# Optimization experiments

Measured on AMD Instinct MI355X. Metric: run time of the kernel, lower is better.

## Reference

```python
import jax, jax.numpy as jnp
import numpy as np
import math

N_PARENT = 60000
CH = 64
BATCH = 2
GRID = 128          # parent voxels on even coords in [0, 256)^3
P_BIT = 0.33
LOG2E = math.log2(math.e)


def _key(b, x, y, z):
    # collision-free int64 key; +4 keeps shifted neighbor coords non-negative
    return ((np.asarray(b, np.int64) * 512 + (x + 4)) * 512 + (y + 4)) * 512 + (z + 4)


def _nbr(qc, tkeys, step):
    # 3x3x3 kernel offset map (torchsparse Conv3d k=3,s=1 at tensor stride `step`)
    so = np.argsort(tkeys)
    sk = tkeys[so]
    d = np.array([-step, 0, step], np.int64)
    offs = np.stack(np.meshgrid(d, d, d, indexing='ij'), -1).reshape(-1, 3)  # [27,3]
    q = _key(qc[:, 0:1], qc[:, 1:2] + offs[None, :, 0],
             qc[:, 2:3] + offs[None, :, 1], qc[:, 3:4] + offs[None, :, 2])
    pos = np.minimum(np.searchsorted(sk, q), len(sk) - 1)
    return np.where(sk[pos] == q, so[pos], -1).astype(np.int32)


def setup_inputs():
    rng = np.random.default_rng(0)
    half = N_PARENT // 2
    cs = []
    for b in range(BATCH):
        lin = rng.choice(GRID ** 3, half, replace=False)
        x, y, z = lin // (GRID * GRID), (lin // GRID) % GRID, lin % GRID
        cs.append(np.stack([np.full(half, b), 2 * x, 2 * y, 2 * z], 1).astype(np.int64))
    C = np.concatenate(cs, 0)                                  # [N,4] batch-major, stride-2 coords
    pkeys = _key(C[:, 0], C[:, 1], C[:, 2], C[:, 3])
    bits1 = rng.random((N_PARENT, 8)) < P_BIT                  # cur_bins[1].F occupancy bits
    bits1[~bits1.any(1), 0] = True
    pidx, bitj = np.nonzero(bits1)                             # row-major order == bool-mask gather order
    off = np.stack([(bitj >> 2) & 1, (bitj >> 1) & 1, bitj & 1], 1)
    CC = np.concatenate([C[pidx, :1], C[pidx, 1:] + off], 1)   # child coords, stride 1
    ckeys = _key(CC[:, 0], CC[:, 1], CC[:, 2], CC[:, 3])
    M = CC.shape[0]
    bits0 = rng.random((M, 8)) < P_BIT                         # cur_bins[0].F
    bits0[~bits0.any(1), 0] = True
    f32 = np.float32

    def lin_(fi, fo):
        return (rng.standard_normal((fi, fo)).astype(f32) / f32(np.sqrt(fi)),
                (rng.standard_normal(fo) * 0.01).astype(f32))

    def conv_(c, d):
        return (rng.standard_normal((27, c, d)).astype(f32) / f32(np.sqrt(27 * c)),
                (rng.standard_normal(d) * 0.01).astype(f32))

    W_dec, b_dec = lin_(CH + 8, CH)
    Wb1, bb1 = conv_(CH, CH)
    Wb2, bb2 = conv_(CH, CH)
    Wp0c, bp0c = conv_(CH, CH)
    Wp0l, bp0l = lin_(CH, CH * 8)
    Wp1c, bp1c = conv_(CH, CH)
    Wp1l, bp1l = lin_(CH, 255)
    a = lambda: np.full((1,), 0.25, f32)   # torch nn.PReLU default
    inp = dict(
        rec_F=rng.standard_normal((N_PARENT, CH)).astype(f32),
        bins1_F=bits1.astype(f32),
        points_num=np.bincount(CC[:, 0], minlength=BATCH).astype(f32),
        W_dec=W_dec, b_dec=b_dec, a_dec=a(),
        Wb1=Wb1, bb1=bb1, ab1=a(), Wb2=Wb2, bb2=bb2, ab2=a(),
        Wp0c=Wp0c, bp0c=bp0c, ap0=a(), Wp0l=Wp0l, bp0l=bp0l,
        Wp1c=Wp1c, bp1c=bp1c, ap1=a(), Wp1l=Wp1l, bp1l=bp1l,
        nbr_rec=_nbr(C, pkeys, 2),
        nbr_child=_nbr(CC, ckeys, 1),
        child_pidx=pidx.astype(np.int32), child_bit=bitj.astype(np.int32),
        bins0=bits0.astype(np.int32),
        oct_kernel=np.arange(7, -1, -1, dtype=np.int32),
        ref_batch=CC[:, 0].astype(np.int32),
    )
    return {k: jnp.asarray(v) for k, v in inp.items()}


def _prelu(x, a):
    return jnp.where(x >= 0, x, a * x)


def _sconv(x, nbr, W, b):
    # sparse 3x3x3 conv: out[i] = b + sum_k W[k]^T x[nbr[i,k]] over existing neighbors
    valid = nbr >= 0
    idx = jnp.maximum(nbr, 0)
    out = jnp.zeros((x.shape[0], W.shape[-1]), x.dtype)
    for k in range(W.shape[0]):  # 27 fixed kernel offsets
        xk = jnp.where(valid[:, k:k + 1], x[idx[:, k]], 0.0)
        out = out + xk @ W[k]
    return out + b


def _forward(rec_F, bins1_F, points_num, W_dec, b_dec, a_dec, Wb1, bb1, ab1, Wb2, bb2, ab2,
             Wp0c, bp0c, ap0, Wp0l, bp0l, Wp1c, bp1c, ap1, Wp1l, bp1l,
             nbr_rec, nbr_child, child_pidx, child_bit, bins0, oct_kernel, ref_batch):
    # pred_steps==2: embed is identity -> embed_f == cur_bins[1].F
    x = jnp.concatenate([rec_F, bins1_F], 1)                  # [N, CH+8]
    h = _prelu(x @ W_dec + b_dec, a_dec)
    # Block: conv-PReLU-conv + residual, PReLU
    t = _prelu(_sconv(h, nbr_rec, Wb1, bb1), ab1)
    t = _sconv(t, nbr_rec, Wb2, bb2) + h
    y = _prelu(t, ab2)                                        # cur_rec.F after dec
    # pred[0]
    p = _prelu(_sconv(y, nbr_rec, Wp0c, bp0c), ap0)
    l8 = (p @ Wp0l + bp0l).reshape(-1, 8, rec_F.shape[1])     # [N,8,CH]
    # bool-mask gather reshape(N,8,CH)[cur_bins[-1].F] -> [M,CH]
    g = l8[child_pidx, child_bit]
    # pred[-1]
    q = _prelu(_sconv(g, nbr_child, Wp1c, bp1c), ap1)
    logits = q @ Wp1l + bp1l                                  # [M,255]
    oct = jnp.sum(bins0 << oct_kernel, axis=1) - 1            # bit-packed targets in [0,254]
    logp = jax.nn.log_softmax(logits, axis=-1)
    ce = -jnp.take_along_axis(logp, oct[:, None], axis=1)[:, 0]
    scattered = points_num[ref_batch]                         # searchsorted+loop == per-batch broadcast
    loss = (ce / scattered).sum() * (LOG2E / points_num.shape[0])
    return y, loss


def reference(rec_F, bins1_F, points_num, W_dec, b_dec, a_dec, Wb1, bb1, ab1, Wb2, bb2, ab2,
              Wp0c, bp0c, ap0, Wp0l, bp0l, Wp1c, bp1c, ap1, Wp1l, bp1l,
              nbr_rec, nbr_child, child_pidx, child_bit, bins0, oct_kernel, ref_batch):
    return _forward(rec_F, bins1_F, points_num, W_dec, b_dec, a_dec, Wb1, bb1, ab1, Wb2, bb2, ab2,
                    Wp0c, bp0c, ap0, Wp0l, bp0l, Wp1c, bp1c, ap1, Wp1l, bp1l,
                    nbr_rec, nbr_child, child_pidx, child_bit, bins0, oct_kernel, ref_batch)
```

## Files before the change

kernel.cpp:

```cpp
#include <hip/hip_runtime.h>
#include <hip/hip_bf16.h>

typedef __hip_bfloat16 bf16;
typedef __attribute__((ext_vector_type(8))) short bf16x8v;
typedef __attribute__((ext_vector_type(4))) float f32x4v;

__device__ __forceinline__ float b2f(bf16 v) { return __bfloat162float(v); }
__device__ __forceinline__ float lo16(unsigned int u) {
    union { unsigned int i; float f; } x; x.i = u << 16; return x.f;
}
__device__ __forceinline__ float hi16(unsigned int u) {
    union { unsigned int i; float f; } x; x.i = u & 0xffff0000u; return x.f;
}
template<typename T>
__device__ __forceinline__ void load8(const T* p, float o[8]);
template<>
__device__ __forceinline__ void load8<bf16>(const bf16* p, float o[8]) {
    uint4 v = *reinterpret_cast<const uint4*>(p);
    o[0] = lo16(v.x); o[1] = hi16(v.x);
    o[2] = lo16(v.y); o[3] = hi16(v.y);
    o[4] = lo16(v.z); o[5] = hi16(v.z);
    o[6] = lo16(v.w); o[7] = hi16(v.w);
}
template<>
__device__ __forceinline__ void load8<float>(const float* p, float o[8]) {
    float4 a = reinterpret_cast<const float4*>(p)[0];
    float4 b = reinterpret_cast<const float4*>(p)[1];
    o[0] = a.x; o[1] = a.y; o[2] = a.z; o[3] = a.w;
    o[4] = b.x; o[5] = b.y; o[6] = b.z; o[7] = b.w;
}

__global__ void k_code(float* __restrict__ out, size_t n, float code)
{
    size_t i0 = (size_t)blockIdx.x * blockDim.x + threadIdx.x;
    size_t stride = (size_t)gridDim.x * blockDim.x;
    for (size_t i = i0; i < n; i += stride) out[i] = code;
}

__global__ __launch_bounds__(256) void k_wt(
    const float* __restrict__ W0, const float* __restrict__ W1,
    const float* __restrict__ W2, const float* __restrict__ W3,
    bf16* __restrict__ WT)
{
    __shared__ float L[64 * 65];
    int wb = blockIdx.x / 27, k = blockIdx.x % 27;
    const float* src = (wb == 0 ? W0 : wb == 1 ? W1 : wb == 2 ? W2 : W3) + (size_t)k * 4096;
    int tid = threadIdx.x;
    #pragma unroll
    for (int i = 0; i < 16; ++i) {
        int e = i * 256 + tid;
        L[(e >> 6) * 65 + (e & 63)] = src[e];
    }
    __syncthreads();
    bf16* dst = WT + ((size_t)wb * 27 + k) * 4096;
    #pragma unroll
    for (int i = 0; i < 16; ++i) {
        int e = i * 256 + tid;
        dst[e] = __float2bfloat16(L[(e & 63) * 65 + (e >> 6)]);
    }
}

__global__ __launch_bounds__(256) void k_wt5(
    const float* __restrict__ W, bf16* __restrict__ WT5)
{
    int c = threadIdx.x;
    #pragma unroll
    for (int j = 0; j < 64; ++j) {
        float v = (c < 255) ? W[(size_t)j * 255 + c] : 0.f;
        WT5[(size_t)c * 64 + j] = __float2bfloat16(v);
    }
}

__global__ __launch_bounds__(256) void k_dec(
    const float* __restrict__ rec, const float* __restrict__ bins,
    const float* __restrict__ W, const float* __restrict__ b, const float* __restrict__ a,
    bf16* __restrict__ h, int N)
{
    __shared__ float Wl[72 * 64];
    int tid = threadIdx.x;
    for (int i = tid; i < 72 * 64; i += 256) Wl[i] = W[i];
    int c = tid & 63, w = tid >> 6;
    float bc = b[c];
    float av = a[0];
    __syncthreads();
    int base = blockIdx.x * 32 + w * 8;
    for (int rr = 0; rr < 8; ++rr) {
        int row = base + rr;
        if (row >= N) break;
        float acc = bc;
        float xv[8];
        #pragma unroll
        for (int j8 = 0; j8 < 8; ++j8) {
            load8(rec + (size_t)row * 64 + j8 * 8, xv);
            int j = j8 * 8;
            #pragma unroll
            for (int t = 0; t < 8; ++t) acc += xv[t] * Wl[(j + t) * 64 + c];
        }
        load8(bins + (size_t)row * 8, xv);
        #pragma unroll
        for (int t = 0; t < 8; ++t) acc += xv[t] * Wl[(64 + t) * 64 + c];
        float v = acc >= 0.f ? acc : av * acc;
        h[(size_t)row * 64 + c] = __float2bfloat16(v);
    }
}

template<int G, bool RES, bool OUTF>
__global__ __launch_bounds__(256) void k_sconv_mfma(
    const bf16* __restrict__ x, const int* __restrict__ nbr,
    const bf16* __restrict__ WT,
    const float* __restrict__ bias, const float* __restrict__ a,
    const bf16* __restrict__ res, bf16* __restrict__ out,
    float* __restrict__ outf, int N)
{
    int tid = threadIdx.x;
    int lane = tid & 63;
    int wv = tid >> 6;
    int l15 = lane & 15;
    int lq = lane >> 4;
    int rowbase = blockIdx.x * (64 * G) + wv * (16 * G);

    f32x4v acc[G][4];
    #pragma unroll
    for (int g = 0; g < G; ++g)
        #pragma unroll
        for (int ct = 0; ct < 4; ++ct) acc[g][ct] = (f32x4v){0.f, 0.f, 0.f, 0.f};

    for (int k = 0; k < 27; ++k) {
        int idx[G];
        int anyl = 0;
        #pragma unroll
        for (int g = 0; g < G; ++g) {
            int row = rowbase + g * 16 + l15;
            idx[g] = (row < N) ? nbr[(size_t)row * 27 + k] : -1;
            anyl |= (idx[g] >= 0) ? 1 : 0;
        }
        if (!__any(anyl)) continue;

        bf16x8v bfr[4][2];
        const bf16* wk = WT + (size_t)k * 4096;
        #pragma unroll
        for (int ct = 0; ct < 4; ++ct) {
            const bf16* wr = wk + (ct * 16 + l15) * 64 + lq * 8;
            bfr[ct][0] = *reinterpret_cast<const bf16x8v*>(wr);
            bfr[ct][1] = *reinterpret_cast<const bf16x8v*>(wr + 32);
        }
        #pragma unroll
        for (int g = 0; g < G; ++g) {
            if (!__any(idx[g] >= 0)) continue;
            bf16x8v a0 = (bf16x8v){0,0,0,0,0,0,0,0};
            bf16x8v a1 = (bf16x8v){0,0,0,0,0,0,0,0};
            if (idx[g] >= 0) {
                const bf16* xr = x + (size_t)idx[g] * 64 + lq * 8;
                a0 = *reinterpret_cast<const bf16x8v*>(xr);
                a1 = *reinterpret_cast<const bf16x8v*>(xr + 32);
            }
            #pragma unroll
            for (int ct = 0; ct < 4; ++ct) {
                acc[g][ct] = __builtin_amdgcn_mfma_f32_16x16x32_bf16(a0, bfr[ct][0], acc[g][ct], 0, 0, 0);
                acc[g][ct] = __builtin_amdgcn_mfma_f32_16x16x32_bf16(a1, bfr[ct][1], acc[g][ct], 0, 0, 0);
            }
        }
    }

    float av = a[0];
    float bs[4];
    #pragma unroll
    for (int ct = 0; ct < 4; ++ct) bs[ct] = bias[ct * 16 + l15];
    #pragma unroll
    for (int g = 0; g < G; ++g) {
        #pragma unroll
        for (int r = 0; r < 4; ++r) {
            int row = rowbase + g * 16 + lq * 4 + r;
            if (row >= N) continue;
            #pragma unroll
            for (int ct = 0; ct < 4; ++ct) {
                int col = ct * 16 + l15;
                float v = acc[g][ct][r] + bs[ct];
                if (RES) v += b2f(res[(size_t)row * 64 + col]);
                v = v >= 0.f ? v : av * v;
                out[(size_t)row * 64 + col] = __float2bfloat16(v);
                if (OUTF) outf[(size_t)row * 64 + col] = v;
            }
        }
    }
}

__global__ __launch_bounds__(256) void k_p0l(
    const bf16* __restrict__ p, const float* __restrict__ W, const float* __restrict__ b,
    const int* __restrict__ pidx, const int* __restrict__ bitj,
    bf16* __restrict__ g, int M)
{
    int tid = threadIdx.x;
    int c = tid & 63, w = tid >> 6;
    int base = blockIdx.x * 32 + w * 8;
    for (int rr = 0; rr < 8; ++rr) {
        int m = base + rr;
        if (m >= M) break;
        int pi = pidx[m];
        int bt = bitj[m];
        int col = bt * 64 + c;
        float acc = b[col];
        float xv[8];
        #pragma unroll
        for (int j8 = 0; j8 < 8; ++j8) {
            load8(p + (size_t)pi * 64 + j8 * 8, xv);
            int j = j8 * 8;
            #pragma unroll
            for (int t = 0; t < 8; ++t)
                acc += xv[t] * W[(size_t)(j + t) * 512 + col];
        }
        g[(size_t)m * 64 + c] = __float2bfloat16(acc);
    }
}

__global__ __launch_bounds__(256) void k_loss_mfma(
    const bf16* __restrict__ q, const bf16* __restrict__ WT5,
    const float* __restrict__ b,
    const int* __restrict__ bins0, const int* __restrict__ octk,
    const int* __restrict__ ref_batch, const float* __restrict__ pn,
    float* __restrict__ accum, int M)
{
    int tid = threadIdx.x;
    int lane = tid & 63;
    int wv = tid >> 6;
    int l15 = lane & 15;
    int lq = lane >> 4;

    bf16x8v bfr[16][2];
    #pragma unroll
    for (int ct = 0; ct < 16; ++ct) {
        const bf16* wr = WT5 + (size_t)(ct * 16 + l15) * 64 + lq * 8;
        bfr[ct][0] = *reinterpret_cast<const bf16x8v*>(wr);
        bfr[ct][1] = *reinterpret_cast<const bf16x8v*>(wr + 32);
    }
    float bs[16];
    #pragma unroll
    for (int ct = 0; ct < 16; ++ct) bs[ct] = (ct * 16 + l15 < 255) ? b[ct * 16 + l15] : 0.f;
    int ok[8];
    #pragma unroll
    for (int j = 0; j < 8; ++j) ok[j] = octk[j];

    float local = 0.f;
    int tiles = (M + 15) / 16;
    int waveId = blockIdx.x * 4 + wv;
    int nWaves = gridDim.x * 4;

    for (int t = waveId; t < tiles; t += nWaves) {
        int rowbase = t * 16;
        int arow = rowbase + l15;
        bf16x8v a0 = (bf16x8v){0,0,0,0,0,0,0,0};
        bf16x8v a1 = (bf16x8v){0,0,0,0,0,0,0,0};
        if (arow < M) {
            const bf16* xr = q + (size_t)arow * 64 + lq * 8;
            a0 = *reinterpret_cast<const bf16x8v*>(xr);
            a1 = *reinterpret_cast<const bf16x8v*>(xr + 32);
        }
        f32x4v acc[16];
        #pragma unroll
        for (int ct = 0; ct < 16; ++ct) {
            f32x4v z = (f32x4v){0.f, 0.f, 0.f, 0.f};
            z = __builtin_amdgcn_mfma_f32_16x16x32_bf16(a0, bfr[ct][0], z, 0, 0, 0);
            z = __builtin_amdgcn_mfma_f32_16x16x32_bf16(a1, bfr[ct][1], z, 0, 0, 0);
            acc[ct] = z;
        }
        #pragma unroll
        for (int ct = 0; ct < 16; ++ct) {
            #pragma unroll
            for (int r = 0; r < 4; ++r) acc[ct][r] += bs[ct];
        }
        #pragma unroll
        for (int r = 0; r < 4; ++r) {
            int row = rowbase + lq * 4 + r;
            bool rv = (row < M);
            int rowc = rv ? row : 0;
            float mx = -1e30f;
            #pragma unroll
            for (int ct = 0; ct < 16; ++ct) {
                float v = acc[ct][r];
                if (ct == 15 && l15 == 15) v = -1e30f;
                mx = fmaxf(mx, v);
            }
            #pragma unroll
            for (int s = 1; s < 16; s <<= 1) mx = fmaxf(mx, __shfl_xor(mx, s, 64));
            float se = 0.f;
            #pragma unroll
            for (int ct = 0; ct < 16; ++ct) {
                if (ct == 15 && l15 == 15) continue;
                se += __expf(acc[ct][r] - mx);
            }
            #pragma unroll
            for (int s = 1; s < 16; s <<= 1) se += __shfl_xor(se, s, 64);
            int oct = 0;
            #pragma unroll
            for (int j = 0; j < 8; ++j) oct += bins0[(size_t)rowc * 8 + j] << ok[j];
            oct -= 1;
            int cts = oct >> 4;
            float cand = acc[0][r];
            #pragma unroll
            for (int ct = 1; ct < 16; ++ct) cand = (cts == ct) ? acc[ct][r] : cand;
            float lo = __shfl(cand, lq * 16 + (oct & 15), 64);
            if (rv && l15 == 0) {
                float ce = mx + __logf(se) - lo;
                local += ce / pn[ref_batch[row]];
            }
        }
    }
    #pragma unroll
    for (int s = 32; s > 0; s >>= 1) local += __shfl_xor(local, s, 64);
    if (lane == 0) atomicAdd(accum, local);
}

__global__ void k_finish(const float* __restrict__ accum, float* __restrict__ outf, int BATCH)
{
    if (threadIdx.x == 0 && blockIdx.x == 0)
        outf[0] = accum[0] * 1.4426950408889634f / (float)BATCH;
}

extern "C" void kernel_launch(void* const* d_in, const int* in_sizes, int n_in,
                              void* d_out, int out_size, void* d_ws, size_t ws_size,
                              hipStream_t stream)
{
    const float* rec_F   = (const float*)d_in[0];
    const float* bins1_F = (const float*)d_in[1];
    const float* pn      = (const float*)d_in[2];
    const float* W_dec   = (const float*)d_in[3];
    const float* b_dec   = (const float*)d_in[4];
    const float* a_dec   = (const float*)d_in[5];
    const float* Wb1     = (const float*)d_in[6];
    const float* bb1     = (const float*)d_in[7];
    const float* ab1     = (const float*)d_in[8];
    const float* Wb2     = (const float*)d_in[9];
    const float* bb2     = (const float*)d_in[10];
    const float* ab2     = (const float*)d_in[11];
    const float* Wp0c    = (const float*)d_in[12];
    const float* bp0c    = (const float*)d_in[13];
    const float* ap0     = (const float*)d_in[14];
    const float* Wp0l    = (const float*)d_in[15];
    const float* bp0l    = (const float*)d_in[16];
    const float* Wp1c    = (const float*)d_in[17];
    const float* bp1c    = (const float*)d_in[18];
    const float* ap1     = (const float*)d_in[19];
    const float* Wp1l    = (const float*)d_in[20];
    const float* bp1l    = (const float*)d_in[21];
    const int* nbr_rec    = (const int*)d_in[22];
    const int* nbr_child  = (const int*)d_in[23];
    const int* child_pidx = (const int*)d_in[24];
    const int* child_bit  = (const int*)d_in[25];
    const int* bins0      = (const int*)d_in[26];
    const int* oct_kernel = (const int*)d_in[27];
    const int* ref_batch  = (const int*)d_in[28];

    int N = in_sizes[0] / 64;
    int M = in_sizes[24];
    int BATCH = in_sizes[2];

    size_t N64 = (size_t)N * 64, M64 = (size_t)M * 64;
    float* out_y    = (float*)d_out;
    float* out_loss = out_y + N64;

    size_t wt_bytes  = (size_t)4 * 27 * 4096 * sizeof(bf16);
    size_t wt5_bytes = (size_t)256 * 64 * sizeof(bf16);
    size_t required = 64 + 4 * M64 + wt_bytes + wt5_bytes;
    if (ws_size < required) {
        float code = 200.f + (float)(ws_size >> 20);
        k_code<<<512, 256, 0, stream>>>(out_y, N64, code);
        k_code<<<1, 64, 0, stream>>>(out_loss, 1, code);
        return;
    }

    char* wsb = (char*)d_ws;
    float* accum = (float*)wsb;
    bf16* buf1 = (bf16*)(wsb + 64);
    bf16* buf2 = buf1 + M64;
    bf16* WT   = buf2 + M64;
    bf16* WT1 = WT;
    bf16* WT2 = WT + (size_t)27 * 4096;
    bf16* WT3 = WT + (size_t)2 * 27 * 4096;
    bf16* WT4 = WT + (size_t)3 * 27 * 4096;
    bf16* WT5 = WT + (size_t)4 * 27 * 4096;

    hipMemsetAsync(wsb, 0, 64, stream);

    k_wt<<<108, 256, 0, stream>>>(Wb1, Wb2, Wp0c, Wp1c, WT);
    k_wt5<<<1, 256, 0, stream>>>(Wp1l, WT5);

    int blocksN32 = (N + 31) / 32;
    int blocksM32 = (M + 31) / 32;
    int blocksN64 = (N + 63) / 64;
    int blocksM256 = (M + 255) / 256;

    k_dec<<<blocksN32, 256, 0, stream>>>(rec_F, bins1_F, W_dec, b_dec, a_dec, buf1, N);

    k_sconv_mfma<1, false, false><<<blocksN64, 256, 0, stream>>>(
        buf1, nbr_rec, WT1, bb1, ab1, nullptr, buf2, nullptr, N);

    k_sconv_mfma<1, true, true><<<blocksN64, 256, 0, stream>>>(
        buf2, nbr_rec, WT2, bb2, ab2, buf1, buf1, out_y, N);

    k_sconv_mfma<1, false, false><<<blocksN64, 256, 0, stream>>>(
        buf1, nbr_rec, WT3, bp0c, ap0, nullptr, buf2, nullptr, N);

    k_p0l<<<blocksM32, 256, 0, stream>>>(buf2, Wp0l, bp0l, child_pidx, child_bit, buf1, M);

    k_sconv_mfma<4, false, false><<<blocksM256, 256, 0, stream>>>(
        buf1, nbr_child, WT4, bp1c, ap1, nullptr, buf2, nullptr, M);

    k_loss_mfma<<<1024, 256, 0, stream>>>(buf2, WT5, bp1l, bins0, oct_kernel,
                                          ref_batch, pn, accum, M);
    k_finish<<<1, 64, 0, stream>>>(accum, out_loss, BATCH);
}
```

Baseline: 611.1 us.

## Rewrite per-child linear layer as bf16 MFMA and stage y output in workspace

The scalar per-child projection kernel, which read fp32 weights from global memory for each output, is replaced by a wave-tiled MFMA kernel. It uses a pre-transposed bf16 weight layout and masks each 16-row tile per child bit, skipping bits absent from the tile. The float y output is now written to a workspace buffer and copied to the output at the end, and the __restrict__ qualifiers on res/out are dropped because those pointers alias. This adds an extra device-to-device copy of N*64 floats plus a small weight-transpose kernel, and each tile may run up to eight masked MFMA passes.

After: 585.7 us. 4.2% less time.

```diff
diff --git a/kernel.cpp b/kernel.cpp
--- a/kernel.cpp
+++ b/kernel.cpp
@@ -68,6 +68,26 @@
     for (int j = 0; j < 64; ++j) {
         float v = (c < 255) ? W[(size_t)j * 255 + c] : 0.f;
         WT5[(size_t)c * 64 + j] = __float2bfloat16(v);
+    }
+}
+
+__global__ __launch_bounds__(256) void k_wtp(
+    const float* __restrict__ W, bf16* __restrict__ WTP)
+{
+    __shared__ float L[64 * 65];
+    int bt = blockIdx.x;
+    int tid = threadIdx.x;
+    #pragma unroll
+    for (int i = 0; i < 16; ++i) {
+        int e = i * 256 + tid;
+        L[(e >> 6) * 65 + (e & 63)] = W[(size_t)(e >> 6) * 512 + bt * 64 + (e & 63)];
+    }
+    __syncthreads();
+    bf16* dst = WTP + (size_t)bt * 4096;
+    #pragma unroll
+    for (int i = 0; i < 16; ++i) {
+        int e = i * 256 + tid;
+        dst[e] = __float2bfloat16(L[(e & 63) * 65 + (e >> 6)]);
     }
 }
 
@@ -109,7 +129,7 @@
     const bf16* __restrict__ x, const int* __restrict__ nbr,
     const bf16* __restrict__ WT,
     const float* __restrict__ bias, const float* __restrict__ a,
-    const bf16* __restrict__ res, bf16* __restrict__ out,
+    const bf16* res, bf16* out,
     float* __restrict__ outf, int N)
 {
     int tid = threadIdx.x;
@@ -185,31 +205,65 @@
     }
 }
 
-__global__ __launch_bounds__(256) void k_p0l(
-    const bf16* __restrict__ p, const float* __restrict__ W, const float* __restrict__ b,
+__global__ __launch_bounds__(256) void k_p0l_mfma(
+    const bf16* __restrict__ p, const bf16* __restrict__ WTP,
+    const float* __restrict__ b,
     const int* __restrict__ pidx, const int* __restrict__ bitj,
     bf16* __restrict__ g, int M)
 {
     int tid = threadIdx.x;
-    int c = tid & 63, w = tid >> 6;
-    int base = blockIdx.x * 32 + w * 8;
-    for (int rr = 0; rr < 8; ++rr) {
-        int m = base + rr;
-        if (m >= M) break;
-        int pi = pidx[m];
-        int bt = bitj[m];
-        int col = bt * 64 + c;
-        float acc = b[col];
-        float xv[8];
-        #pragma unroll
-        for (int j8 = 0; j8 < 8; ++j8) {
-            load8(p + (size_t)pi * 64 + j8 * 8, xv);
-            int j = j8 * 8;
-            #pragma unroll
-            for (int t = 0; t < 8; ++t)
-                acc += xv[t] * W[(size_t)(j + t) * 512 + col];
-        }
-        g[(size_t)m * 64 + c] = __float2bfloat16(acc);
+    int lane = tid & 63;
+    int wv = tid >> 6;
+    int l15 = lane & 15;
+    int lq = lane >> 4;
+    int tiles = (M + 15) / 16;
+    int waveId = blockIdx.x * 4 + wv;
+    int nWaves = gridDim.x * 4;
+    const bf16x8v zv = (bf16x8v){0,0,0,0,0,0,0,0};
+
+    for (int t = waveId; t < tiles; t += nWaves) {
+        int rowbase = t * 16;
+        int m = rowbase + l15;
+        bool mv = (m < M);
+        int pi = mv ? pidx[m] : 0;
+        int bt = mv ? bitj[m] : -1;
+        bf16x8v a0 = zv, a1 = zv;
+        if (mv) {
+            const bf16* xr = p + (size_t)pi * 64 + lq * 8;
+            a0 = *reinterpret_cast<const bf16x8v*>(xr);
+            a1 = *reinterpret_cast<const bf16x8v*>(xr + 32);
+        }
+        f32x4v acc[4];
+        #pragma unroll
+        for (int ct = 0; ct < 4; ++ct) acc[ct] = (f32x4v){0.f, 0.f, 0.f, 0.f};
+
+        #pragma unroll
+        for (int b8 = 0; b8 < 8; ++b8) {
+            if (!__any(bt == b8)) continue;
+            bf16x8v m0 = (bt == b8) ? a0 : zv;
+            bf16x8v m1 = (bt == b8) ? a1 : zv;
+            const bf16* wk = WTP + (size_t)b8 * 4096;
+            #pragma unroll
+            for (int ct = 0; ct < 4; ++ct) {
+                const bf16* wr = wk + (ct * 16 + l15) * 64 + lq * 8;
+                bf16x8v b0 = *reinterpret_cast<const bf16x8v*>(wr);
+                bf16x8v b1 = *reinterpret_cast<const bf16x8v*>(wr + 32);
+                acc[ct] = __builtin_amdgcn_mfma_f32_16x16x32_bf16(m0, b0, acc[ct], 0, 0, 0);
+                acc[ct] = __builtin_amdgcn_mfma_f32_16x16x32_bf16(m1, b1, acc[ct], 0, 0, 0);
+            }
+        }
+        #pragma unroll
+        for (int r = 0; r < 4; ++r) {
+            int row = rowbase + lq * 4 + r;
+            if (row >= M) continue;
+            int btr = bitj[row];
+            #pragma unroll
+            for (int ct = 0; ct < 4; ++ct) {
+                int col = ct * 16 + l15;
+                float v = acc[ct][r] + b[btr * 64 + col];
+                g[(size_t)row * 64 + col] = __float2bfloat16(v);
+            }
+        }
     }
 }
 
@@ -360,7 +414,9 @@
 
     size_t wt_bytes  = (size_t)4 * 27 * 4096 * sizeof(bf16);
     size_t wt5_bytes = (size_t)256 * 64 * sizeof(bf16);
-    size_t required = 64 + 4 * M64 + wt_bytes + wt5_bytes;
+    size_t wtp_bytes = (size_t)8 * 4096 * sizeof(bf16);
+    size_t yf_bytes  = 4 * N64;
+    size_t required = 64 + 4 * M64 + yf_bytes + wt_bytes + wt5_bytes + wtp_bytes;
     if (ws_size < required) {
         float code = 200.f + (float)(ws_size >> 20);
         k_code<<<512, 256, 0, stream>>>(out_y, N64, code);
@@ -372,20 +428,22 @@
     float* accum = (float*)wsb;
     bf16* buf1 = (bf16*)(wsb + 64);
     bf16* buf2 = buf1 + M64;
-    bf16* WT   = buf2 + M64;
+    float* yf  = (float*)(buf2 + M64);
+    bf16* WT   = (bf16*)((char*)yf + yf_bytes);
     bf16* WT1 = WT;
     bf16* WT2 = WT + (size_t)27 * 4096;
     bf16* WT3 = WT + (size_t)2 * 27 * 4096;
     bf16* WT4 = WT + (size_t)3 * 27 * 4096;
     bf16* WT5 = WT + (size_t)4 * 27 * 4096;
+    bf16* WTP = WT5 + (size_t)256 * 64;
 
     hipMemsetAsync(wsb, 0, 64, stream);
 
     k_wt<<<108, 256, 0, stream>>>(Wb1, Wb2, Wp0c, Wp1c, WT);
     k_wt5<<<1, 256, 0, stream>>>(Wp1l, WT5);
+    k_wtp<<<8, 256, 0, stream>>>(Wp0l, WTP);
 
     int blocksN32 = (N + 31) / 32;
-    int blocksM32 = (M + 31) / 32;
     int blocksN64 = (N + 63) / 64;
     int blocksM256 = (M + 255) / 256;
 
@@ -395,12 +453,12 @@
         buf1, nbr_rec, WT1, bb1, ab1, nullptr, buf2, nullptr, N);
 
     k_sconv_mfma<1, true, true><<<blocksN64, 256, 0, stream>>>(
-        buf2, nbr_rec, WT2, bb2, ab2, buf1, buf1, out_y, N);
+        buf2, nbr_rec, WT2, bb2, ab2, buf1, buf1, yf, N);
 
     k_sconv_mfma<1, false, false><<<blocksN64, 256, 0, stream>>>(
         buf1, nbr_rec, WT3, bp0c, ap0, nullptr, buf2, nullptr, N);
 
-    k_p0l<<<blocksM32, 256, 0, stream>>>(buf2, Wp0l, bp0l, child_pidx, child_bit, buf1, M);
+    k_p0l_mfma<<<1024, 256, 0, stream>>>(buf2, WTP, bp0l, child_pidx, child_bit, buf1, M);
 
     k_sconv_mfma<4, false, false><<<blocksM256, 256, 0, stream>>>(
         buf1, nbr_child, WT4, bp1c, ap1, nullptr, buf2, nullptr, M);
@@ -408,4 +466,6 @@
     k_loss_mfma<<<1024, 256, 0, stream>>>(buf2, WT5, bp1l, bins0, oct_kernel,
                                           ref_batch, pn, accum, M);
     k_finish<<<1, 64, 0, stream>>>(accum, out_loss, BATCH);
-}
+
+    hipMemcpyAsync(out_y, yf, yf_bytes, hipMemcpyDeviceToDevice, stream);
+}
```
